# Kernel tuning notes

Hardware: AMD Instinct MI355X
Metric: run time of the kernel (lower is better)

The kernel has to match this reference:

```python
import jax, jax.numpy as jnp
import numpy as np

N_BLOCKS = 96
N = N_BLOCKS ** 2          # number of image blocks = n_blocks^2
D = 1024                   # feature dim (fixed by Linear(1024+1, 128))
EPS_COS = 1e-6             # eps of F.cosine_similarity
EPS_BN = 1e-5              # BatchNorm1d eps


def setup_inputs() -> dict:
    key = jax.random.key(0)
    ks = jax.random.split(key, 6)
    return {
        "features": jax.random.normal(ks[0], (N, D), dtype=jnp.float32),
        "scores": jax.random.uniform(ks[1], (N,), dtype=jnp.float32),
        "W1": jax.random.normal(ks[2], (D + 1, 128), dtype=jnp.float32) * 0.03,
        "b1": jnp.zeros((128,), jnp.float32),
        "g1": jnp.ones((128,), jnp.float32),
        "be1": jnp.zeros((128,), jnp.float32),
        "W2": jax.random.normal(ks[3], (128, 64), dtype=jnp.float32) * 0.08,
        "b2": jnp.zeros((64,), jnp.float32),
        "g2": jnp.ones((64,), jnp.float32),
        "be2": jnp.zeros((64,), jnp.float32),
        "W3": jax.random.normal(ks[4], (64, 1), dtype=jnp.float32) * 0.12,
        "b3": jnp.zeros((1,), jnp.float32),
    }


def _gaussian_similarity(features):
    # Vectorized form of the O(N^2) pairwise loop:
    #   cos_ij = <f_i, f_j> / max(|f_i||f_j|, eps)
    #   sigma^2 = D * (0.5 + 0.5 * cos)  ->  2*sigma^2 = D * (1 + cos)
    #   sim_ij = exp(-|f_i - f_j|^2 / (2*sigma^2)),  sim_ii = 1
    sq = jnp.sum(features * features, axis=-1)          # [N] squared norms
    gram = features @ features.T                          # [N, N] big GEMM
    norms = jnp.sqrt(sq)
    cos = gram / jnp.maximum(norms[:, None] * norms[None, :], EPS_COS)
    d2 = jnp.maximum(sq[:, None] + sq[None, :] - 2.0 * gram, 0.0)
    denom = jnp.maximum(jnp.float32(D) * (1.0 + cos), EPS_COS)
    sim = jnp.exp(-d2 / denom)
    eye = jnp.eye(sim.shape[0], dtype=bool)
    return jnp.where(eye, jnp.float32(1.0), sim)


def _bn_eval(h, gamma, beta):
    # BatchNorm1d in eval mode with init running stats (mean=0, var=1).
    return gamma * (h / jnp.sqrt(1.0 + EPS_BN)) + beta


def reference(features, scores, W1, b1, g1, be1, W2, b2, g2, be2, W3, b3):
    sim = _gaussian_similarity(features)                  # [N, N]
    x = jnp.concatenate([features, scores[:, None]], axis=1)  # [N, D+1]
    h = jax.nn.relu(_bn_eval(x @ W1 + b1, g1, be1))       # [N, 128]
    h = jax.nn.relu(_bn_eval(h @ W2 + b2, g2, be2))       # [N, 64]
    agg = jax.nn.sigmoid(h @ W3 + b3)[:, 0]               # [N]
    sim_mean = jnp.mean(sim, axis=1)                      # [N]
    # Torch broadcast [N,1] * [N] -> [N,N], then .mean() == mean(agg)*mean(sim_mean)
    return jnp.mean(agg) * jnp.mean(sim_mean)


if __name__ == "__main__":
    out = reference(**setup_inputs())
    print(out)
```

## Files before the change

kernel.cpp:

```cpp
#include <hip/hip_runtime.h>

#define N_IMG 9216
#define DFEAT 1024
#define NBC 36
#define NBR 72
#define NPAIR 1332

typedef __attribute__((ext_vector_type(8))) short short8;
typedef __attribute__((ext_vector_type(4))) float floatx4;
typedef __attribute__((ext_vector_type(16))) float floatx16;
typedef __attribute__((ext_vector_type(4))) int intx4;
typedef __attribute__((ext_vector_type(8))) int intx8;

__device__ __forceinline__ void async_copy16(const void* g, void* l) {
  __builtin_amdgcn_global_load_lds((const __attribute__((address_space(1))) void*)g,
                                   (__attribute__((address_space(3))) void*)l,
                                   16, 0, 0);
}

__device__ __forceinline__ unsigned short f2bf(float x) {
  union { float f; unsigned u; } a; a.f = x;
  unsigned u = a.u;
  u += 0x7fffu + ((u >> 16) & 1u);
  return (unsigned short)(u >> 16);
}

__device__ __forceinline__ size_t sw_decode(int P) {
  int L = P >> 3, ix = (P & 7) ^ (L & 7);
  return (size_t)(L * 2 + (ix >> 2)) * DFEAT + (size_t)(ix & 3) * 16;
}

__device__ __forceinline__ intx4 ld16s(const unsigned char* base, int r, int c) {
  int L = r >> 1, ix = (((r & 1) << 2) | c) ^ (L & 7);
  return *(const intx4*)(base + L * 128 + ix * 16);
}

__device__ __forceinline__ intx8 ldfrags(const unsigned char* base, int r, int kh) {
  intx4 lo = ld16s(base, r, kh * 2);
  intx4 hi = ld16s(base, r, kh * 2 + 1);
  intx8 v;
  v[0] = lo[0]; v[1] = lo[1]; v[2] = lo[2]; v[3] = lo[3];
  v[4] = hi[0]; v[5] = hi[1]; v[6] = hi[2]; v[7] = hi[3];
  return v;
}

__global__ __launch_bounds__(256) void convert_prep(const float* __restrict__ f,
                                                    const float* __restrict__ W1,
                                                    unsigned char* __restrict__ fb8,
                                                    float* __restrict__ sq,
                                                    float* __restrict__ rn,
                                                    unsigned short* __restrict__ W1t,
                                                    double* __restrict__ sums) {
  int b = blockIdx.x, t = threadIdx.x;
  if (b < 2304) {
    int lane = t & 63, wave = t >> 6;
    int row = b * 4 + wave;
    const float4* src = (const float4*)f + (size_t)row * 256;
    unsigned int* dst = (unsigned int*)(fb8 + (size_t)row * DFEAT);
    float s = 0.f;
#pragma unroll
    for (int j = 0; j < 4; j++) {
      float4 v = src[j * 64 + lane];
      s += v.x * v.x + v.y * v.y + v.z * v.z + v.w * v.w;
      int pk = __builtin_amdgcn_cvt_pk_fp8_f32(v.x, v.y, 0, false);
      pk = __builtin_amdgcn_cvt_pk_fp8_f32(v.z, v.w, pk, true);
      dst[j * 64 + lane] = (unsigned int)pk;
    }
#pragma unroll
    for (int off = 32; off > 0; off >>= 1) s += __shfl_down(s, off, 64);
    if (lane == 0) { sq[row] = s; rn[row] = rsqrtf(s); }
  } else {
    int j = b - 2304;
    if (j == 0 && t < 2) sums[t] = 0.0;
    for (int k = t; k < DFEAT; k += 256)
      W1t[(size_t)j * DFEAT + k] = f2bf(W1[(size_t)k * 128 + j]);
  }
}

__global__ __launch_bounds__(256, 2) void gram_sim(const unsigned char* __restrict__ fb8,
                                                   const float* __restrict__ sq,
                                                   const float* __restrict__ rn,
                                                   double* __restrict__ sums) {
  int rem = blockIdx.x, bcol = 0;
  for (;;) {
    int m = 2 * bcol + 2; if (m > NBR) m = NBR;
    if (rem < m) break;
    rem -= m; bcol++;
  }
  int brow = rem;

  __shared__ __align__(16) unsigned char Ab[2][8192];
  __shared__ __align__(16) unsigned char Bb[2][16384];
  __shared__ float sqA[128], rnA[128], sqB[256], rnB[256];
  __shared__ float wpart[4];

  int t = threadIdx.x, lane = t & 63, wave = t >> 6;
  if (t < 128) { sqA[t] = sq[brow * 128 + t]; rnA[t] = rn[brow * 128 + t]; }
  sqB[t] = sq[bcol * 256 + t];
  rnB[t] = rn[bcol * 256 + t];

  const unsigned char* Asrc = fb8 + (size_t)brow * 128 * DFEAT;
  const unsigned char* Bsrc = fb8 + (size_t)bcol * 256 * DFEAT;

  const size_t d0 = sw_decode(t);
  const size_t d1 = sw_decode(t + 256);
  const size_t d2 = sw_decode(t + 512);
  const size_t d3 = sw_decode(t + 768);

  floatx16 acc[2][4];
#pragma unroll
  for (int mi = 0; mi < 2; mi++)
#pragma unroll
    for (int ni = 0; ni < 4; ni++)
#pragma unroll
      for (int e = 0; e < 16; e++) acc[mi][ni][e] = 0.f;

  const int wr = (wave & 1) * 64, wc = (wave >> 1) * 128;
  const int r32 = lane & 31, kh = lane >> 5;

  async_copy16(Asrc + d0, &Ab[0][t * 16]);
  async_copy16(Asrc + d1, &Ab[0][(t + 256) * 16]);
  async_copy16(Bsrc + d0, &Bb[0][t * 16]);
  async_copy16(Bsrc + d1, &Bb[0][(t + 256) * 16]);
  async_copy16(Bsrc + d2, &Bb[0][(t + 512) * 16]);
  async_copy16(Bsrc + d3, &Bb[0][(t + 768) * 16]);

  for (int kb = 0; kb < 16; kb++) {
    __syncthreads();
    if (kb < 15) {
      const int nb = (kb + 1) & 1;
      const size_t k0 = (size_t)(kb + 1) * 64;
      async_copy16(Asrc + d0 + k0, &Ab[nb][t * 16]);
      async_copy16(Asrc + d1 + k0, &Ab[nb][(t + 256) * 16]);
      async_copy16(Bsrc + d0 + k0, &Bb[nb][t * 16]);
      async_copy16(Bsrc + d1 + k0, &Bb[nb][(t + 256) * 16]);
      async_copy16(Bsrc + d2 + k0, &Bb[nb][(t + 512) * 16]);
      async_copy16(Bsrc + d3 + k0, &Bb[nb][(t + 768) * 16]);
    }
    const unsigned char* Ac = Ab[kb & 1];
    const unsigned char* Bc = Bb[kb & 1];
    intx8 a[2], b[4];
#pragma unroll
    for (int mi = 0; mi < 2; mi++) a[mi] = ldfrags(Ac, wr + mi * 32 + r32, kh);
#pragma unroll
    for (int ni = 0; ni < 4; ni++) b[ni] = ldfrags(Bc, wc + ni * 32 + r32, kh);
#pragma unroll
    for (int mi = 0; mi < 2; mi++)
#pragma unroll
      for (int ni = 0; ni < 4; ni++)
        acc[mi][ni] = __builtin_amdgcn_mfma_scale_f32_32x32x64_f8f6f4(
            a[mi], b[ni], acc[mi][ni], 0, 0, 0, 0x7F7F7F7F, 0, 0x7F7F7F7F);
  }

  const bool interior = (brow < 2 * bcol);
  float lsum = 0.f;
#pragma unroll
  for (int ni = 0; ni < 4; ni++) {
    int j_loc = wc + ni * 32 + r32;
    float sj = sqB[j_loc], rnj = rnB[j_loc];
    int j_g = bcol * 256 + j_loc;
#pragma unroll
    for (int mi = 0; mi < 2; mi++) {
      int rbase = wr + mi * 32 + 4 * kh;
#pragma unroll
      for (int reg = 0; reg < 16; reg++) {
        int i_loc = rbase + (reg & 3) + 8 * (reg >> 2);
        float gv = acc[mi][ni][reg];
        float si = sqA[i_loc], rni = rnA[i_loc];
        float cosv = gv * rni * rnj;
        float den = fmaf(1024.f, cosv, 1024.f);
        float d2 = si + sj - (gv + gv);
        float sim = __builtin_amdgcn_exp2f(-d2 * __builtin_amdgcn_rcpf(den) * 1.44269504f);
        if (interior) {
          lsum += sim;
        } else {
          int i_g = brow * 128 + i_loc;
          lsum += (i_g < j_g) ? 2.f * sim : (i_g == j_g ? 1.f : 0.f);
        }
      }
    }
  }
  if (interior) lsum *= 2.f;
#pragma unroll
  for (int off = 32; off > 0; off >>= 1) lsum += __shfl_down(lsum, off, 64);
  if (lane == 0) wpart[wave] = lsum;
  __syncthreads();
  if (t == 0)
    atomicAdd(&sums[0], (double)(wpart[0] + wpart[1] + wpart[2] + wpart[3]));
}

__global__ __launch_bounds__(256) void mlp_full(const float* __restrict__ f,
                                                const unsigned short* __restrict__ W1t,
                                                const float* __restrict__ scores,
                                                const float* __restrict__ W1,
                                                const float* __restrict__ b1,
                                                const float* __restrict__ g1,
                                                const float* __restrict__ be1,
                                                const float* __restrict__ W2, const float* __restrict__ b2,
                                                const float* __restrict__ g2, const float* __restrict__ be2,
                                                const float* __restrict__ W3, const float* __restrict__ b3,
                                                double* __restrict__ sums) {
  int r0 = blockIdx.x * 64;

  __shared__ __align__(16) float As32[64 * 32];
  __shared__ __align__(16) unsigned short Bs[128 * 32];
  __shared__ float h1s[64][128];
  __shared__ float h2s[64][65];
  __shared__ float sc[64], b1s[128], g1s[128], be1s[128], wls[128], ls[64];

  int t = threadIdx.x, lane = t & 63, wave = t >> 6;
  if (t < 64) sc[t] = scores[r0 + t];
  if (t < 128) {
    b1s[t] = b1[t]; g1s[t] = g1[t]; be1s[t] = be1[t];
    wls[t] = W1[(size_t)DFEAT * 128 + t];
  }

  floatx4 acc[2][4];
#pragma unroll
  for (int a = 0; a < 2; a++)
#pragma unroll
    for (int b = 0; b < 4; b++) acc[a][b] = (floatx4){0.f, 0.f, 0.f, 0.f};

  const int wr = (wave & 1) * 32, wc = (wave >> 1) * 64;

  for (int k0 = 0; k0 < DFEAT; k0 += 32) {
    __syncthreads();
    {
      int c = t, rA = c >> 3, p = c & 7, l = p ^ (rA & 7);
      async_copy16(f + (size_t)(r0 + rA) * DFEAT + k0 + l * 4, (char*)As32 + c * 16);
      c = t + 256; rA = c >> 3; p = c & 7; l = p ^ (rA & 7);
      async_copy16(f + (size_t)(r0 + rA) * DFEAT + k0 + l * 4, (char*)As32 + c * 16);
      c = t; int rB = c >> 2; p = c & 3; l = p ^ (rB & 3);
      async_copy16(W1t + (size_t)rB * DFEAT + k0 + l * 8, (char*)Bs + c * 16);
      c = t + 256; rB = c >> 2; p = c & 3; l = p ^ (rB & 3);
      async_copy16(W1t + (size_t)rB * DFEAT + k0 + l * 8, (char*)Bs + c * 16);
    }
    __syncthreads();

    const int mrow = lane & 15, kq = (lane >> 4) * 8;
    short8 a[2], b[4];
#pragma unroll
    for (int mt = 0; mt < 2; mt++) {
      int row = wr + mt * 16 + mrow;
      int l0 = kq >> 2;
      int p0 = l0 ^ (row & 7), p1 = (l0 + 1) ^ (row & 7);
      float4 f0 = *(const float4*)&As32[row * 32 + p0 * 4];
      float4 f1 = *(const float4*)&As32[row * 32 + p1 * 4];
      short8 af;
      af[0] = (short)f2bf(f0.x); af[1] = (short)f2bf(f0.y);
      af[2] = (short)f2bf(f0.z); af[3] = (short)f2bf(f0.w);
      af[4] = (short)f2bf(f1.x); af[5] = (short)f2bf(f1.y);
      af[6] = (short)f2bf(f1.z); af[7] = (short)f2bf(f1.w);
      a[mt] = af;
    }
#pragma unroll
    for (int nt = 0; nt < 4; nt++) {
      int row = wc + nt * 16 + mrow;
      int p = (kq >> 3) ^ (row & 3);
      b[nt] = *(const short8*)&Bs[row * 32 + p * 8];
    }
#pragma unroll
    for (int mt = 0; mt < 2; mt++)
#pragma unroll
      for (int nt = 0; nt < 4; nt++)
        acc[mt][nt] = __builtin_amdgcn_mfma_f32_16x16x32_bf16(a[mt], b[nt], acc[mt][nt], 0, 0, 0);
  }

  const float inv = 1.0f / sqrtf(1.0f + 1e-5f);
  const int rq = (lane >> 4) * 4, cn = lane & 15;
#pragma unroll
  for (int nt = 0; nt < 4; nt++) {
    int j = wc + nt * 16 + cn;
    float bj = b1s[j], gj = g1s[j] * inv, bej = be1s[j], wj = wls[j];
#pragma unroll
    for (int mt = 0; mt < 2; mt++) {
#pragma unroll
      for (int rr = 0; rr < 4; rr++) {
        int iL = wr + mt * 16 + rq + rr;
        float pre = acc[mt][nt][rr] + sc[iL] * wj + bj;
        h1s[iL][j] = fmaxf(gj * pre + bej, 0.f);
      }
    }
  }
  __syncthreads();

  {
    int j = t & 63, rg = (t >> 6) * 16;
    float a2[16];
#pragma unroll
    for (int rr = 0; rr < 16; rr++) a2[rr] = 0.f;
    for (int k = 0; k < 128; k++) {
      float w = W2[k * 64 + j];
#pragma unroll
      for (int rr = 0; rr < 16; rr++) a2[rr] = fmaf(h1s[rg + rr][k], w, a2[rr]);
    }
    float scv = g2[j] * inv, bi = b2[j], be = be2[j];
#pragma unroll
    for (int rr = 0; rr < 16; rr++)
      h2s[rg + rr][j] = fmaxf(scv * (a2[rr] + bi) + be, 0.f);
  }
  __syncthreads();

  if (t < 64) {
    float z = b3[0];
#pragma unroll
    for (int k = 0; k < 64; k++) z = fmaf(h2s[t][k], W3[k], z);
    ls[t] = 1.f / (1.f + __expf(-z));
  }
  __syncthreads();
  if (t == 0) {
    float s = 0.f;
#pragma unroll
    for (int iL = 0; iL < 64; iL++) s += ls[iL];
    atomicAdd(&sums[1], (double)s);
  }
}

__global__ void finalize(const double* __restrict__ sums, float* __restrict__ out) {
  double simmean = sums[0] / ((double)N_IMG * (double)N_IMG);
  double aggmean = sums[1] / (double)N_IMG;
  out[0] = (float)(aggmean * simmean);
}

extern "C" void kernel_launch(void* const* d_in, const int* in_sizes, int n_in,
                              void* d_out, int out_size, void* d_ws, size_t ws_size,
                              hipStream_t stream) {
  const float* f      = (const float*)d_in[0];
  const float* scores = (const float*)d_in[1];
  const float* W1 = (const float*)d_in[2];
  const float* b1 = (const float*)d_in[3];
  const float* g1 = (const float*)d_in[4];
  const float* be1 = (const float*)d_in[5];
  const float* W2 = (const float*)d_in[6];
  const float* b2 = (const float*)d_in[7];
  const float* g2 = (const float*)d_in[8];
  const float* be2 = (const float*)d_in[9];
  const float* W3 = (const float*)d_in[10];
  const float* b3 = (const float*)d_in[11];

  char* ws = (char*)d_ws;
  unsigned char* fb8  = (unsigned char*)ws;
  float* sq           = (float*)(ws + 9437184);
  float* rn           = (float*)(ws + 9474048);
  unsigned short* W1t = (unsigned short*)(ws + 9510912);
  double* sums        = (double*)(ws + 9773056);

  convert_prep<<<2432, 256, 0, stream>>>(f, W1, fb8, sq, rn, W1t, sums);
  gram_sim<<<NPAIR, 256, 0, stream>>>(fb8, sq, rn, sums);
  mlp_full<<<144, 256, 0, stream>>>(f, W1t, scores, W1, b1, g1, be1,
                                    W2, b2, g2, be2, W3, b3, sums);
  finalize<<<1, 1, 0, stream>>>(sums, (float*)d_out);
}
```

Before: 204.5 us.

## Normalize FP8 features, simplify similarity epilogue, change LDS swizzle, halve MLP tiles

Features are pre-normalized by their norm before the FP8 conversion, so the GEMM yields cosine directly. The Gaussian exponent is refactored into one reciprocal of (1+cos) plus an FMA using per-row precomputed constants, which cuts epilogue ALU work. The LDS swizzle for the FP8 tiles changes from XOR to a rotation pattern. The MLP kernel uses 32-row tiles with twice as many blocks for more parallelism. Quantizing normalized vectors changes FP8 rounding behaviour, and the new swizzle must stay consistent between the write and read sides.

```diff
diff --git a/kernel.cpp b/kernel.cpp
--- a/kernel.cpp
+++ b/kernel.cpp
@@ -2,7 +2,6 @@
 
 #define N_IMG 9216
 #define DFEAT 1024
-#define NBC 36
 #define NBR 72
 #define NPAIR 1332
 
@@ -12,6 +11,9 @@
 typedef __attribute__((ext_vector_type(4))) int intx4;
 typedef __attribute__((ext_vector_type(8))) int intx8;
 
+#define C1F 0.0014088818759657845f
+#define C2F 0.05308355472172724f
+
 __device__ __forceinline__ void async_copy16(const void* g, void* l) {
   __builtin_amdgcn_global_load_lds((const __attribute__((address_space(1))) void*)g,
                                    (__attribute__((address_space(3))) void*)l,
@@ -25,16 +27,17 @@
   return (unsigned short)(u >> 16);
 }
 
-__device__ __forceinline__ size_t sw_decode(int P) {
-  int L = P >> 3, ix = (P & 7) ^ (L & 7);
-  return (size_t)(L * 2 + (ix >> 2)) * DFEAT + (size_t)(ix & 3) * 16;
-}
-
+__device__ __forceinline__ size_t sw_src(int P) {
+  int L = P >> 3, s = P & 7;
+  int row = 2 * L + (s & 1);
+  int c = ((s >> 1) - L) & 3;
+  return (size_t)row * DFEAT + (size_t)c * 16;
+}
 __device__ __forceinline__ intx4 ld16s(const unsigned char* base, int r, int c) {
-  int L = r >> 1, ix = (((r & 1) << 2) | c) ^ (L & 7);
-  return *(const intx4*)(base + L * 128 + ix * 16);
-}
-
+  int L = r >> 1;
+  int slot = (((c + L) & 3) << 1) | (r & 1);
+  return *(const intx4*)(base + L * 128 + slot * 16);
+}
 __device__ __forceinline__ intx8 ldfrags(const unsigned char* base, int r, int kh) {
   intx4 lo = ld16s(base, r, kh * 2);
   intx4 hi = ld16s(base, r, kh * 2 + 1);
@@ -47,8 +50,8 @@
 __global__ __launch_bounds__(256) void convert_prep(const float* __restrict__ f,
                                                     const float* __restrict__ W1,
                                                     unsigned char* __restrict__ fb8,
-                                                    float* __restrict__ sq,
-                                                    float* __restrict__ rn,
+                                                    float* __restrict__ sL,
+                                                    float* __restrict__ pL,
                                                     unsigned short* __restrict__ W1t,
                                                     double* __restrict__ sums) {
   int b = blockIdx.x, t = threadIdx.x;
@@ -57,18 +60,26 @@
     int row = b * 4 + wave;
     const float4* src = (const float4*)f + (size_t)row * 256;
     unsigned int* dst = (unsigned int*)(fb8 + (size_t)row * DFEAT);
-    float s = 0.f;
+    float4 v0 = src[lane], v1 = src[64 + lane], v2 = src[128 + lane], v3 = src[192 + lane];
+    float s = v0.x * v0.x + v0.y * v0.y + v0.z * v0.z + v0.w * v0.w
+            + v1.x * v1.x + v1.y * v1.y + v1.z * v1.z + v1.w * v1.w
+            + v2.x * v2.x + v2.y * v2.y + v2.z * v2.z + v2.w * v2.w
+            + v3.x * v3.x + v3.y * v3.y + v3.z * v3.z + v3.w * v3.w;
+#pragma unroll
+    for (int off = 32; off > 0; off >>= 1) s += __shfl_xor(s, off, 64);
+    float rinv = rsqrtf(s);
+    float4 vv[4] = {v0, v1, v2, v3};
 #pragma unroll
     for (int j = 0; j < 4; j++) {
-      float4 v = src[j * 64 + lane];
-      s += v.x * v.x + v.y * v.y + v.z * v.z + v.w * v.w;
-      int pk = __builtin_amdgcn_cvt_pk_fp8_f32(v.x, v.y, 0, false);
-      pk = __builtin_amdgcn_cvt_pk_fp8_f32(v.z, v.w, pk, true);
+      float4 v = vv[j];
+      int pk = __builtin_amdgcn_cvt_pk_fp8_f32(v.x * rinv, v.y * rinv, 0, false);
+      pk = __builtin_amdgcn_cvt_pk_fp8_f32(v.z * rinv, v.w * rinv, pk, true);
       dst[j * 64 + lane] = (unsigned int)pk;
     }
-#pragma unroll
-    for (int off = 32; off > 0; off >>= 1) s += __shfl_down(s, off, 64);
-    if (lane == 0) { sq[row] = s; rn[row] = rsqrtf(s); }
+    if (lane == 0) {
+      sL[row] = s * C1F;
+      pL[row] = sqrtf(s) * C2F;
+    }
   } else {
     int j = b - 2304;
     if (j == 0 && t < 2) sums[t] = 0.0;
@@ -78,34 +89,34 @@
 }
 
 __global__ __launch_bounds__(256, 2) void gram_sim(const unsigned char* __restrict__ fb8,
-                                                   const float* __restrict__ sq,
-                                                   const float* __restrict__ rn,
+                                                   const float* __restrict__ sL,
+                                                   const float* __restrict__ pL,
                                                    double* __restrict__ sums) {
   int rem = blockIdx.x, bcol = 0;
   for (;;) {
-    int m = 2 * bcol + 2; if (m > NBR) m = NBR;
-    if (rem < m) break;
-    rem -= m; bcol++;
+    int mlim = 2 * bcol + 2; if (mlim > NBR) mlim = NBR;
+    if (rem < mlim) break;
+    rem -= mlim; bcol++;
   }
   int brow = rem;
 
   __shared__ __align__(16) unsigned char Ab[2][8192];
   __shared__ __align__(16) unsigned char Bb[2][16384];
-  __shared__ float sqA[128], rnA[128], sqB[256], rnB[256];
+  __shared__ float sA[128], pA[128], sB[256], pB[256];
   __shared__ float wpart[4];
 
   int t = threadIdx.x, lane = t & 63, wave = t >> 6;
-  if (t < 128) { sqA[t] = sq[brow * 128 + t]; rnA[t] = rn[brow * 128 + t]; }
-  sqB[t] = sq[bcol * 256 + t];
-  rnB[t] = rn[bcol * 256 + t];
+  if (t < 128) { sA[t] = sL[brow * 128 + t]; pA[t] = pL[brow * 128 + t]; }
+  sB[t] = sL[bcol * 256 + t];
+  pB[t] = pL[bcol * 256 + t];
 
   const unsigned char* Asrc = fb8 + (size_t)brow * 128 * DFEAT;
   const unsigned char* Bsrc = fb8 + (size_t)bcol * 256 * DFEAT;
 
-  const size_t d0 = sw_decode(t);
-  const size_t d1 = sw_decode(t + 256);
-  const size_t d2 = sw_decode(t + 512);
-  const size_t d3 = sw_decode(t + 768);
+  const size_t d0 = sw_src(t);
+  const size_t d1 = sw_src(t + 256);
+  const size_t d2 = sw_src(t + 512);
+  const size_t d3 = sw_src(t + 768);
 
   floatx16 acc[2][4];
 #pragma unroll
@@ -153,28 +164,40 @@
   }
 
   const bool interior = (brow < 2 * bcol);
-  float lsum = 0.f;
+  float sjv[4], pjv[4];
 #pragma unroll
   for (int ni = 0; ni < 4; ni++) {
     int j_loc = wc + ni * 32 + r32;
-    float sj = sqB[j_loc], rnj = rnB[j_loc];
-    int j_g = bcol * 256 + j_loc;
-#pragma unroll
-    for (int mi = 0; mi < 2; mi++) {
-      int rbase = wr + mi * 32 + 4 * kh;
-#pragma unroll
-      for (int reg = 0; reg < 16; reg++) {
-        int i_loc = rbase + (reg & 3) + 8 * (reg >> 2);
-        float gv = acc[mi][ni][reg];
-        float si = sqA[i_loc], rni = rnA[i_loc];
-        float cosv = gv * rni * rnj;
-        float den = fmaf(1024.f, cosv, 1024.f);
-        float d2 = si + sj - (gv + gv);
-        float sim = __builtin_amdgcn_exp2f(-d2 * __builtin_amdgcn_rcpf(den) * 1.44269504f);
-        if (interior) {
-          lsum += sim;
-        } else {
-          int i_g = brow * 128 + i_loc;
+    sjv[ni] = sB[j_loc];
+    pjv[ni] = pB[j_loc];
+  }
+  float lsum = 0.f;
+#pragma unroll
+  for (int mi = 0; mi < 2; mi++) {
+    const int rbase = wr + mi * 32 + 4 * kh;
+#pragma unroll
+    for (int reg = 0; reg < 16; reg++) {
+      const int i_loc = rbase + (reg & 3) + 8 * (reg >> 2);
+      const float si = sA[i_loc], pi = pA[i_loc];
+      if (interior) {
+#pragma unroll
+        for (int ni = 0; ni < 4; ni++) {
+          float u = acc[mi][ni][reg];
+          float r = __builtin_amdgcn_rcpf(1.f + u);
+          float del = pi * pjv[ni];
+          float gam = si + sjv[ni] + del;
+          lsum += __builtin_amdgcn_exp2f(fmaf(-gam, r, del));
+        }
+      } else {
+        int i_g = brow * 128 + i_loc;
+#pragma unroll
+        for (int ni = 0; ni < 4; ni++) {
+          int j_g = bcol * 256 + wc + ni * 32 + r32;
+          float u = acc[mi][ni][reg];
+          float r = __builtin_amdgcn_rcpf(1.f + u);
+          float del = pi * pjv[ni];
+          float gam = si + sjv[ni] + del;
+          float sim = __builtin_amdgcn_exp2f(fmaf(-gam, r, del));
           lsum += (i_g < j_g) ? 2.f * sim : (i_g == j_g ? 1.f : 0.f);
         }
       }
@@ -200,37 +223,33 @@
                                                 const float* __restrict__ g2, const float* __restrict__ be2,
                                                 const float* __restrict__ W3, const float* __restrict__ b3,
                                                 double* __restrict__ sums) {
-  int r0 = blockIdx.x * 64;
-
-  __shared__ __align__(16) float As32[64 * 32];
+  int r0 = blockIdx.x * 32;
+
+  __shared__ __align__(16) float As32[32 * 32];
   __shared__ __align__(16) unsigned short Bs[128 * 32];
-  __shared__ float h1s[64][128];
-  __shared__ float h2s[64][65];
-  __shared__ float sc[64], b1s[128], g1s[128], be1s[128], wls[128], ls[64];
+  __shared__ float h1s[32][128];
+  __shared__ float h2s[32][65];
+  __shared__ float sc[32], b1s[128], g1s[128], be1s[128], wls[128], ls[32];
 
   int t = threadIdx.x, lane = t & 63, wave = t >> 6;
-  if (t < 64) sc[t] = scores[r0 + t];
+  if (t < 32) sc[t] = scores[r0 + t];
   if (t < 128) {
     b1s[t] = b1[t]; g1s[t] = g1[t]; be1s[t] = be1[t];
     wls[t] = W1[(size_t)DFEAT * 128 + t];
   }
 
-  floatx4 acc[2][4];
-#pragma unroll
-  for (int a = 0; a < 2; a++)
-#pragma unroll
-    for (int b = 0; b < 4; b++) acc[a][b] = (floatx4){0.f, 0.f, 0.f, 0.f};
-
-  const int wr = (wave & 1) * 32, wc = (wave >> 1) * 64;
+  floatx4 acc[4];
+#pragma unroll
+  for (int b = 0; b < 4; b++) acc[b] = (floatx4){0.f, 0.f, 0.f, 0.f};
+
+  const int wr = (wave & 1) * 16, wc = (wave >> 1) * 64;
 
   for (int k0 = 0; k0 < DFEAT; k0 += 32) {
     __syncthreads();
     {
-      int c = t, rA = c >> 3, p = c & 7, l = p ^ (rA & 7);
-      async_copy16(f + (size_t)(r0 + rA) * DFEAT + k0 + l * 4, (char*)As32 + c * 16);
-      c = t + 256; rA = c >> 3; p = c & 7; l = p ^ (rA & 7);
-      async_copy16(f + (size_t)(r0 + rA) * DFEAT + k0 + l * 4, (char*)As32 + c * 16);
-      c = t; int rB = c >> 2; p = c & 3; l = p ^ (rB & 3);
+      int rA = t >> 3, p = t & 7, l = p ^ (rA & 7);
+      async_copy16(f + (size_t)(r0 + rA) * DFEAT + k0 + l * 4, (char*)As32 + t * 16);
+      int c = t, rB = c >> 2; p = c & 3; l = p ^ (rB & 3);
       async_copy16(W1t + (size_t)rB * DFEAT + k0 + l * 8, (char*)Bs + c * 16);
       c = t + 256; rB = c >> 2; p = c & 3; l = p ^ (rB & 3);
       async_copy16(W1t + (size_t)rB * DFEAT + k0 + l * 8, (char*)Bs + c * 16);
@@ -238,20 +257,17 @@
     __syncthreads();
 
     const int mrow = lane & 15, kq = (lane >> 4) * 8;
-    short8 a[2], b[4];
-#pragma unroll
-    for (int mt = 0; mt < 2; mt++) {
-      int row = wr + mt * 16 + mrow;
+    short8 a, b[4];
+    {
+      int row = wr + mrow;
       int l0 = kq >> 2;
       int p0 = l0 ^ (row & 7), p1 = (l0 + 1) ^ (row & 7);
       float4 f0 = *(const float4*)&As32[row * 32 + p0 * 4];
       float4 f1 = *(const float4*)&As32[row * 32 + p1 * 4];
-      short8 af;
-      af[0] = (short)f2bf(f0.x); af[1] = (short)f2bf(f0.y);
-      af[2] = (short)f2bf(f0.z); af[3] = (short)f2bf(f0.w);
-      af[4] = (short)f2bf(f1.x); af[5] = (short)f2bf(f1.y);
-      af[6] = (short)f2bf(f1.z); af[7] = (short)f2bf(f1.w);
-      a[mt] = af;
+      a[0] = (short)f2bf(f0.x); a[1] = (short)f2bf(f0.y);
+      a[2] = (short)f2bf(f0.z); a[3] = (short)f2bf(f0.w);
+      a[4] = (short)f2bf(f1.x); a[5] = (short)f2bf(f1.y);
+      a[6] = (short)f2bf(f1.z); a[7] = (short)f2bf(f1.w);
     }
 #pragma unroll
     for (int nt = 0; nt < 4; nt++) {
@@ -260,10 +276,8 @@
       b[nt] = *(const short8*)&Bs[row * 32 + p * 8];
     }
 #pragma unroll
-    for (int mt = 0; mt < 2; mt++)
-#pragma unroll
-      for (int nt = 0; nt < 4; nt++)
-        acc[mt][nt] = __builtin_amdgcn_mfma_f32_16x16x32_bf16(a[mt], b[nt], acc[mt][nt], 0, 0, 0);
+    for (int nt = 0; nt < 4; nt++)
+      acc[nt] = __builtin_amdgcn_mfma_f32_16x16x32_bf16(a, b[nt], acc[nt], 0, 0, 0);
   }
 
   const float inv = 1.0f / sqrtf(1.0f + 1e-5f);
@@ -273,35 +287,32 @@
     int j = wc + nt * 16 + cn;
     float bj = b1s[j], gj = g1s[j] * inv, bej = be1s[j], wj = wls[j];
 #pragma unroll
-    for (int mt = 0; mt < 2; mt++) {
-#pragma unroll
-      for (int rr = 0; rr < 4; rr++) {
-        int iL = wr + mt * 16 + rq + rr;
-        float pre = acc[mt][nt][rr] + sc[iL] * wj + bj;
-        h1s[iL][j] = fmaxf(gj * pre + bej, 0.f);
-      }
+    for (int rr = 0; rr < 4; rr++) {
+      int iL = wr + rq + rr;
+      float pre = acc[nt][rr] + sc[iL] * wj + bj;
+      h1s[iL][j] = fmaxf(gj * pre + bej, 0.f);
     }
   }
   __syncthreads();
 
   {
-    int j = t & 63, rg = (t >> 6) * 16;
-    float a2[16];
-#pragma unroll
-    for (int rr = 0; rr < 16; rr++) a2[rr] = 0.f;
+    int j = t & 63, rg = (t >> 6) * 8;
+    float a2[8];
+#pragma unroll
+    for (int rr = 0; rr < 8; rr++) a2[rr] = 0.f;
     for (int k = 0; k < 128; k++) {
       float w = W2[k * 64 + j];
 #pragma unroll
-      for (int rr = 0; rr < 16; rr++) a2[rr] = fmaf(h1s[rg + rr][k], w, a2[rr]);
+      for (int rr = 0; rr < 8; rr++) a2[rr] = fmaf(h1s[rg + rr][k], w, a2[rr]);
     }
     float scv = g2[j] * inv, bi = b2[j], be = be2[j];
 #pragma unroll
-    for (int rr = 0; rr < 16; rr++)
+    for (int rr = 0; rr < 8; rr++)
       h2s[rg + rr][j] = fmaxf(scv * (a2[rr] + bi) + be, 0.f);
   }
   __syncthreads();
 
-  if (t < 64) {
+  if (t < 32) {
     float z = b3[0];
 #pragma unroll
     for (int k = 0; k < 64; k++) z = fmaf(h2s[t][k], W3[k], z);
@@ -311,7 +322,7 @@
   if (t == 0) {
     float s = 0.f;
 #pragma unroll
-    for (int iL = 0; iL < 64; iL++) s += ls[iL];
+    for (int iL = 0; iL < 32; iL++) s += ls[iL];
     atomicAdd(&sums[1], (double)s);
   }
 }
@@ -340,14 +351,14 @@
 
   char* ws = (char*)d_ws;
   unsigned char* fb8  = (unsigned char*)ws;
-  float* sq           = (float*)(ws + 9437184);
-  float* rn           = (float*)(ws + 9474048);
+  float* sL           = (float*)(ws + 9437184);
+  float* pL           = (float*)(ws + 9474048);
   unsigned short* W1t = (unsigned short*)(ws + 9510912);
   double* sums        = (double*)(ws + 9773056);
 
-  convert_prep<<<2432, 256, 0, stream>>>(f, W1, fb8, sq, rn, W1t, sums);
-  gram_sim<<<NPAIR, 256, 0, stream>>>(fb8, sq, rn, sums);
-  mlp_full<<<144, 256, 0, stream>>>(f, W1t, scores, W1, b1, g1, be1,
+  convert_prep<<<2432, 256, 0, stream>>>(f, W1, fb8, sL, pL, W1t, sums);
+  gram_sim<<<NPAIR, 256, 0, stream>>>(fb8, sL, pL, sums);
+  mlp_full<<<288, 256, 0, stream>>>(f, W1t, scores, W1, b1, g1, be1,
                                     W2, b2, g2, be2, W3, b3, sums);
   finalize<<<1, 1, 0, stream>>>(sums, (float*)d_out);
 }
```

New measurement: 457.0 us. 124% more time.
